# Performance work log

Hardware: AMD Instinct MI355X
Metric: run time of the kernel (lower is better)

Reference implementation:

```python
import jax, jax.numpy as jnp
import numpy as np

N = 50000
E = 800000
IN_DIM = 128
HIDDEN = 96
HEADS = 4
HEAD_DIM = HIDDEN // HEADS
NUM_LAYERS = 3
NEG_SLOPE = 0.2


def _gat_layer(h, W, a_l, a_r, b, src, dst):
    # h: [N, F_in], W: [F_in, H*D], a_l/a_r: [H, D], b: [H, D]
    feat = (h @ W).reshape(N, HEADS, HEAD_DIM)          # [N, H, D]
    el = jnp.sum(feat * a_l, axis=-1)                    # [N, H]
    er = jnp.sum(feat * a_r, axis=-1)                    # [N, H]
    e = el[src] + er[dst]                                # [E, H]
    e = jnp.where(e > 0, e, NEG_SLOPE * e)               # leaky_relu
    # edge softmax over incoming edges of each dst node
    m = jax.ops.segment_max(e, dst, num_segments=N)      # [N, H]
    ex = jnp.exp(e - m[dst])                             # [E, H]
    denom = jax.ops.segment_sum(ex, dst, num_segments=N) # [N, H]
    alpha = ex / denom[dst]                              # [E, H]
    msg = feat[src] * alpha[:, :, None]                  # [E, H, D]
    out = jax.ops.segment_sum(msg, dst, num_segments=N)  # [N, H, D]
    out = out + b                                        # bias
    out = jax.nn.elu(out)                                # activation
    return out.reshape(N, HEADS * HEAD_DIM)              # flatten(1)


def setup_inputs() -> dict:
    key = jax.random.key(0)
    ks = jax.random.split(key, 16)
    feats = jax.random.normal(ks[0], (N, IN_DIM), dtype=jnp.float32)
    src = jax.random.randint(ks[1], (E,), 0, N)
    dst = jax.random.randint(ks[2], (E,), 0, N)
    inp = {"feats": feats, "src": src, "dst": dst}
    fin = IN_DIM
    for l in range(NUM_LAYERS):
        s = 1.0 / np.sqrt(fin)
        inp[f"W{l}"] = jax.random.normal(ks[3 + 4 * l], (fin, HIDDEN), dtype=jnp.float32) * s
        inp[f"al{l}"] = jax.random.normal(ks[4 + 4 * l], (HEADS, HEAD_DIM), dtype=jnp.float32) * 0.1
        inp[f"ar{l}"] = jax.random.normal(ks[5 + 4 * l], (HEADS, HEAD_DIM), dtype=jnp.float32) * 0.1
        inp[f"b{l}"] = jnp.zeros((HEADS, HEAD_DIM), dtype=jnp.float32)
        fin = HIDDEN
    return inp


def reference(feats, src, dst, W0, al0, ar0, b0, W1, al1, ar1, b1, W2, al2, ar2, b2):
    h = feats
    params = [(W0, al0, ar0, b0), (W1, al1, ar1, b1), (W2, al2, ar2, b2)]
    for (W, al, ar, b) in params:
        h = _gat_layer(h, W, al, ar, b, src, dst)
    # AvgPooling over all nodes (single graph) -> [1, HIDDEN]
    return jnp.mean(h, axis=0, keepdims=True)
```

## Files before the change

### kernel.cpp

```cpp
#include <hip/hip_runtime.h>
#include <hip/hip_bf16.h>

#define N_NODES 50000
#define E_EDGES 800000
#define IN_DIM  128
#define HIDDEN  96
#define HEADS   4
#define HEAD_DIM 24
#define NEG_SLOPE 0.2f
#define POOL_BLOCKS 256


__global__ void k_hist(const int* __restrict__ dst, int* __restrict__ deg) {
    int e = blockIdx.x * 256 + threadIdx.x;
    if (e < E_EDGES) atomicAdd(&deg[dst[e]], 1);
}

__global__ __launch_bounds__(256) void k_scan1(const int* __restrict__ deg,
                                               int* __restrict__ bsum, int n) {
    int i = blockIdx.x * 256 + threadIdx.x;
    int v = (i < n) ? deg[i] : 0;
#pragma unroll
    for (int s = 1; s < 64; s <<= 1) v += __shfl_xor(v, s);
    __shared__ int ws[4];
    if ((threadIdx.x & 63) == 0) ws[threadIdx.x >> 6] = v;
    __syncthreads();
    if (threadIdx.x == 0) bsum[blockIdx.x] = ws[0] + ws[1] + ws[2] + ws[3];
}

__global__ __launch_bounds__(256) void k_scan3(const int* __restrict__ deg,
                                               const int* __restrict__ bsum,
                                               int* __restrict__ off, int n) {
    int tid = threadIdx.x;
    int lane = tid & 63, wv = tid >> 6;

    int pv = (tid < blockIdx.x) ? bsum[tid] : 0;
#pragma unroll
    for (int s = 1; s < 64; s <<= 1) pv += __shfl_xor(pv, s);

    int i = blockIdx.x * 256 + tid;
    int v = (i < n) ? deg[i] : 0;
    int x = v;
#pragma unroll
    for (int s = 1; s < 64; s <<= 1) {
        int t = __shfl_up(x, s);
        if (lane >= s) x += t;
    }

    __shared__ int wsum[4], wsum2[4];
    if (lane == 63) wsum[wv] = x;
    if (lane == 0)  wsum2[wv] = pv;
    __syncthreads();
    int add = wsum2[0] + wsum2[1] + wsum2[2] + wsum2[3];
    for (int w = 0; w < wv; ++w) add += wsum[w];
    if (i < n) off[i] = x - v + add;
    if (i == n - 1) off[n] = x + add;
}

__global__ void k_fill(const int* __restrict__ src, const int* __restrict__ dst,
                       const int* __restrict__ off, int* __restrict__ cursor,
                       int* __restrict__ ssrc) {
    int e = blockIdx.x * 256 + threadIdx.x;
    if (e < E_EDGES) {
        int d = dst[e];
        int p = off[d] + atomicAdd(&cursor[d], 1);
        ssrc[p] = src[e];
    }
}


template <int K>
__global__ __launch_bounds__(384) void k_gemm(const float* __restrict__ h,
                                              const float* __restrict__ W,
                                              const float* __restrict__ al_g,
                                              const float* __restrict__ ar_g,
                                              float* __restrict__ feat,
                                              float* __restrict__ el,
                                              float* __restrict__ er, int n) {
    constexpr int HL = 64 * K;
    constexpr int PT = 384 * 17;
    constexpr int SM = (HL > PT) ? HL : PT;
    __shared__ float smem[SM];
    float* hl = smem;

    int node0 = blockIdx.x * 64;
    int total4 = 64 * K / 4;
    for (int idx = threadIdx.x; idx < total4; idx += 384) {
        int node = idx / (K / 4);
        int koff = (idx % (K / 4)) * 4;
        float4 v = make_float4(0.f, 0.f, 0.f, 0.f);
        if (node0 + node < n)
            v = *(const float4*)(&h[(size_t)(node0 + node) * K + koff]);
        *(float4*)(&hl[node * K + koff]) = v;
    }
    __syncthreads();
    int grp = threadIdx.x / 48;
    int c = (threadIdx.x % 48) * 2;
    int nb = grp * 8;
    float acc[8][2];
#pragma unroll
    for (int i = 0; i < 8; ++i) acc[i][0] = acc[i][1] = 0.f;
    for (int k = 0; k < K; k += 4) {
        float2 w0 = *(const float2*)&W[(k + 0) * 96 + c];
        float2 w1 = *(const float2*)&W[(k + 1) * 96 + c];
        float2 w2 = *(const float2*)&W[(k + 2) * 96 + c];
        float2 w3 = *(const float2*)&W[(k + 3) * 96 + c];
#pragma unroll
        for (int i = 0; i < 8; ++i) {
            float4 hv = *(const float4*)&hl[(nb + i) * K + k];
            acc[i][0] = fmaf(hv.x, w0.x, acc[i][0]);
            acc[i][1] = fmaf(hv.x, w0.y, acc[i][1]);
            acc[i][0] = fmaf(hv.y, w1.x, acc[i][0]);
            acc[i][1] = fmaf(hv.y, w1.y, acc[i][1]);
            acc[i][0] = fmaf(hv.z, w2.x, acc[i][0]);
            acc[i][1] = fmaf(hv.z, w2.y, acc[i][1]);
            acc[i][0] = fmaf(hv.w, w3.x, acc[i][0]);
            acc[i][1] = fmaf(hv.w, w3.y, acc[i][1]);
        }
    }
#pragma unroll
    for (int i = 0; i < 8; ++i) {
        int node = node0 + nb + i;
        if (node < n) *(float2*)&feat[(size_t)node * 96 + c] = make_float2(acc[i][0], acc[i][1]);
    }
    float alc0 = al_g[c], alc1 = al_g[c + 1];
    float arc0 = ar_g[c], arc1 = ar_g[c + 1];
    __syncthreads();
    float* part = smem;
    int base = threadIdx.x * 17;
#pragma unroll
    for (int i = 0; i < 8; ++i) {
        part[base + i * 2]     = acc[i][0] * alc0 + acc[i][1] * alc1;
        part[base + i * 2 + 1] = acc[i][0] * arc0 + acc[i][1] * arc1;
    }
    __syncthreads();
    if (threadIdx.x < 256) {
        int ig = threadIdx.x >> 2;
        int hh = threadIdx.x & 3;
        int g2 = ig >> 3, il = ig & 7;
        float se = 0.f, sr = 0.f;
#pragma unroll
        for (int cc = 0; cc < 12; ++cc) {
            int t = g2 * 48 + hh * 12 + cc;
            se += part[t * 17 + il * 2];
            sr += part[t * 17 + il * 2 + 1];
        }
        int node = node0 + ig;
        if (node < n) {
            el[node * 4 + hh] = se;
            er[node * 4 + hh] = sr;
        }
    }
}

__global__ __launch_bounds__(256) void k_agg(const int* __restrict__ off,
                                             const int* __restrict__ ssrc,
                                             const float* __restrict__ el,
                                             const float* __restrict__ er,
                                             const float* __restrict__ feat,
                                             const float* __restrict__ bias,
                                             float* __restrict__ out) {
    int n = blockIdx.x * 4 + (threadIdx.x >> 6);
    if (n >= N_NODES) return;
    int lane = threadIdx.x & 63;
    int j0   = lane >> 3;
    int h    = (lane >> 1) & 3;
    int half = lane & 1;
    int cbase = h * 24 + half * 12;
    unsigned cboff = (unsigned)cbase * 4u;

    int start = off[n], deg = off[n + 1] - start;
    float er_h = er[(unsigned)n * 4u + h];

    float e_reg[4];
    unsigned s_reg[4];
    float lmax = -1e30f;
#pragma unroll
    for (int t = 0; t < 4; ++t) {
        int j = t * 8 + j0;
        bool act = (j < deg);
        unsigned s = act ? (unsigned)ssrc[start + j] : 0u;
        float e = -1e30f;
        if (act) {
            e = el[s * 4u + h] + er_h;
            e = (e > 0.f) ? e : NEG_SLOPE * e;
        }
        s_reg[t] = s;
        e_reg[t] = e;
        lmax = fmaxf(lmax, e);
    }
    for (int j = 32 + j0; j < deg; j += 8) {
        unsigned s = (unsigned)ssrc[start + j];
        float e = el[s * 4u + h] + er_h;
        e = (e > 0.f) ? e : NEG_SLOPE * e;
        lmax = fmaxf(lmax, e);
    }
    lmax = fmaxf(lmax, __shfl_xor(lmax, 8));
    lmax = fmaxf(lmax, __shfl_xor(lmax, 16));
    lmax = fmaxf(lmax, __shfl_xor(lmax, 32));
    float m = lmax;

    float acc[12];
#pragma unroll
    for (int c = 0; c < 12; ++c) acc[c] = 0.f;
    float den = 0.f;
#pragma unroll
    for (int t = 0; t < 4; ++t) {
        int j = t * 8 + j0;
        if (j < deg) {
            float ex = __expf(e_reg[t] - m);
            den += ex;
            const float* fr = (const float*)((const char*)feat + (size_t)(s_reg[t] * 384u + cboff));
            float4 v0 = *(const float4*)(fr + 0);
            float4 v1 = *(const float4*)(fr + 4);
            float4 v2 = *(const float4*)(fr + 8);
            acc[0] = fmaf(ex, v0.x, acc[0]);  acc[1] = fmaf(ex, v0.y, acc[1]);
            acc[2] = fmaf(ex, v0.z, acc[2]);  acc[3] = fmaf(ex, v0.w, acc[3]);
            acc[4] = fmaf(ex, v1.x, acc[4]);  acc[5] = fmaf(ex, v1.y, acc[5]);
            acc[6] = fmaf(ex, v1.z, acc[6]);  acc[7] = fmaf(ex, v1.w, acc[7]);
            acc[8] = fmaf(ex, v2.x, acc[8]);  acc[9] = fmaf(ex, v2.y, acc[9]);
            acc[10] = fmaf(ex, v2.z, acc[10]); acc[11] = fmaf(ex, v2.w, acc[11]);
        }
    }
    for (int j = 32 + j0; j < deg; j += 8) {
        unsigned s = (unsigned)ssrc[start + j];
        float e = el[s * 4u + h] + er_h;
        e = (e > 0.f) ? e : NEG_SLOPE * e;
        float ex = __expf(e - m);
        den += ex;
        const float* fr = (const float*)((const char*)feat + (size_t)(s * 384u + cboff));
        float4 v0 = *(const float4*)(fr + 0);
        float4 v1 = *(const float4*)(fr + 4);
        float4 v2 = *(const float4*)(fr + 8);
        acc[0] = fmaf(ex, v0.x, acc[0]);  acc[1] = fmaf(ex, v0.y, acc[1]);
        acc[2] = fmaf(ex, v0.z, acc[2]);  acc[3] = fmaf(ex, v0.w, acc[3]);
        acc[4] = fmaf(ex, v1.x, acc[4]);  acc[5] = fmaf(ex, v1.y, acc[5]);
        acc[6] = fmaf(ex, v1.z, acc[6]);  acc[7] = fmaf(ex, v1.w, acc[7]);
        acc[8] = fmaf(ex, v2.x, acc[8]);  acc[9] = fmaf(ex, v2.y, acc[9]);
        acc[10] = fmaf(ex, v2.z, acc[10]); acc[11] = fmaf(ex, v2.w, acc[11]);
    }

#pragma unroll
    for (int st = 8; st <= 32; st <<= 1) {
        den += __shfl_xor(den, st);
#pragma unroll
        for (int c = 0; c < 12; ++c) acc[c] += __shfl_xor(acc[c], st);
    }

    if (j0 == 0) {
        float rden = (den > 0.f) ? 1.f / den : 0.f;
        const float* bp = &bias[cbase];
        float o[12];
#pragma unroll
        for (int c = 0; c < 12; ++c) {
            float v = acc[c] * rden + bp[c];
            o[c] = (v > 0.f) ? v : (__expf(v) - 1.f);
        }
        float* op = &out[(size_t)n * 96 + cbase];
        *(float4*)(op + 0) = make_float4(o[0], o[1], o[2], o[3]);
        *(float4*)(op + 4) = make_float4(o[4], o[5], o[6], o[7]);
        *(float4*)(op + 8) = make_float4(o[8], o[9], o[10], o[11]);
    }
}

__global__ __launch_bounds__(384) void k_pool1(const float* __restrict__ h,
                                               float* __restrict__ partial) {
    int r = threadIdx.x / 96;
    int c = threadIdx.x % 96;
    float a = 0.f;
    for (int nrow = blockIdx.x * 4 + r; nrow < N_NODES; nrow += POOL_BLOCKS * 4)
        a += h[(size_t)nrow * 96 + c];
    __shared__ float sred[4][96];
    sred[r][c] = a;
    __syncthreads();
    if (r == 0)
        partial[blockIdx.x * 96 + c] = sred[0][c] + sred[1][c] + sred[2][c] + sred[3][c];
}

__global__ __launch_bounds__(384) void k_pool2(const float* __restrict__ partial,
                                               float* __restrict__ out) {
    int g = threadIdx.x / 96;
    int c = threadIdx.x % 96;
    float a = 0.f;
    for (int b = g; b < POOL_BLOCKS; b += 4)
        a += partial[b * 96 + c];
    __shared__ float sred[4][96];
    sred[g][c] = a;
    __syncthreads();
    if (g == 0)
        out[c] = (sred[0][c] + sred[1][c] + sred[2][c] + sred[3][c]) * (1.0f / N_NODES);
}


extern "C" void kernel_launch(void* const* d_in, const int* in_sizes, int n_in,
                              void* d_out, int out_size, void* d_ws, size_t ws_size,
                              hipStream_t stream) {
    const float* feats = (const float*)d_in[0];
    const int* src = (const int*)d_in[1];
    const int* dst = (const int*)d_in[2];

    char* p = (char*)d_ws;
    auto alloc = [&](size_t bytes) {
        void* r = (void*)p;
        p += (bytes + 255) & ~(size_t)255;
        return r;
    };
    float* A       = (float*)alloc((size_t)N_NODES * 96 * 4);
    float* B       = (float*)alloc((size_t)N_NODES * 96 * 4);
    float* el      = (float*)alloc((size_t)N_NODES * 4 * 4);
    float* er      = (float*)alloc((size_t)N_NODES * 4 * 4);
    int* degcur    = (int*)alloc((size_t)N_NODES * 2 * 4);
    int* off       = (int*)alloc((size_t)(N_NODES + 1) * 4);
    int* bsum      = (int*)alloc((size_t)256 * 4);
    int* ssrc      = (int*)alloc((size_t)E_EDGES * 4);
    float* partial = (float*)alloc((size_t)POOL_BLOCKS * 96 * 4);
    int* deg = degcur;
    int* cursor = degcur + N_NODES;

    hipMemsetAsync(degcur, 0, (size_t)N_NODES * 2 * 4, stream);

    const int NB = (N_NODES + 255) / 256;
    k_hist<<<(E_EDGES + 255) / 256, 256, 0, stream>>>(dst, deg);
    k_scan1<<<NB, 256, 0, stream>>>(deg, bsum, N_NODES);
    k_scan3<<<NB, 256, 0, stream>>>(deg, bsum, off, N_NODES);
    k_fill<<<(E_EDGES + 255) / 256, 256, 0, stream>>>(src, dst, off, cursor, ssrc);

    const float* hin = feats;
    for (int l = 0; l < 3; ++l) {
        const float* W  = (const float*)d_in[3 + 4 * l];
        const float* al = (const float*)d_in[4 + 4 * l];
        const float* ar = (const float*)d_in[5 + 4 * l];
        const float* bb = (const float*)d_in[6 + 4 * l];

        if (l == 0)
            k_gemm<IN_DIM><<<(N_NODES + 63) / 64, 384, 0, stream>>>(hin, W, al, ar, B, el, er, N_NODES);
        else
            k_gemm<HIDDEN><<<(N_NODES + 63) / 64, 384, 0, stream>>>(hin, W, al, ar, B, el, er, N_NODES);

        k_agg<<<(N_NODES + 3) / 4, 256, 0, stream>>>(off, ssrc, el, er, B, bb, A);
        hin = A;
    }

    k_pool1<<<POOL_BLOCKS, 384, 0, stream>>>(A, partial);
    k_pool2<<<1, 384, 0, stream>>>(partial, (float*)d_out);
}
```

Before: 439.5 us.

## Store projected features in fp16 and merge scan and pooling kernels

The projected features written by the GEMM are stored as fp16 and converted back to float in the aggregation kernel, which halves the bytes gathered per edge. The two-pass scan is folded into one kernel in which each block re-sums all earlier degrees. The two-stage pooling reduction is replaced by atomic adds into an output that the histogram kernel zeroes first. This removes two launches at the cost of fp16 rounding error, redundant prefix reads and non-deterministic float atomics.

New measurement: 420.5 us. 1.05x faster.

```diff
diff --git a/kernel.cpp b/kernel.cpp
--- a/kernel.cpp
+++ b/kernel.cpp
@@ -1,44 +1,31 @@
 #include <hip/hip_runtime.h>
-#include <hip/hip_bf16.h>
+#include <hip/hip_fp16.h>
 
 #define N_NODES 50000
 #define E_EDGES 800000
 #define IN_DIM  128
 #define HIDDEN  96
-#define HEADS   4
-#define HEAD_DIM 24
 #define NEG_SLOPE 0.2f
 #define POOL_BLOCKS 256
 
 
-__global__ void k_hist(const int* __restrict__ dst, int* __restrict__ deg) {
+__global__ void k_hist(const int* __restrict__ dst, int* __restrict__ deg,
+                       float* __restrict__ out) {
+    if (blockIdx.x == 0 && threadIdx.x < 96) out[threadIdx.x] = 0.f;
     int e = blockIdx.x * 256 + threadIdx.x;
     if (e < E_EDGES) atomicAdd(&deg[dst[e]], 1);
 }
 
-__global__ __launch_bounds__(256) void k_scan1(const int* __restrict__ deg,
-                                               int* __restrict__ bsum, int n) {
-    int i = blockIdx.x * 256 + threadIdx.x;
-    int v = (i < n) ? deg[i] : 0;
-#pragma unroll
-    for (int s = 1; s < 64; s <<= 1) v += __shfl_xor(v, s);
-    __shared__ int ws[4];
-    if ((threadIdx.x & 63) == 0) ws[threadIdx.x >> 6] = v;
-    __syncthreads();
-    if (threadIdx.x == 0) bsum[blockIdx.x] = ws[0] + ws[1] + ws[2] + ws[3];
-}
-
-__global__ __launch_bounds__(256) void k_scan3(const int* __restrict__ deg,
-                                               const int* __restrict__ bsum,
-                                               int* __restrict__ off, int n) {
+__global__ __launch_bounds__(256) void k_scan(const int* __restrict__ deg,
+                                              int* __restrict__ off, int n) {
     int tid = threadIdx.x;
     int lane = tid & 63, wv = tid >> 6;
-
-    int pv = (tid < blockIdx.x) ? bsum[tid] : 0;
+    int base = blockIdx.x * 256;
+    int pv = 0;
+    for (int i = tid; i < base; i += 256) pv += deg[i];
 #pragma unroll
     for (int s = 1; s < 64; s <<= 1) pv += __shfl_xor(pv, s);
-
-    int i = blockIdx.x * 256 + tid;
+    int i = base + tid;
     int v = (i < n) ? deg[i] : 0;
     int x = v;
 #pragma unroll
@@ -46,12 +33,11 @@
         int t = __shfl_up(x, s);
         if (lane >= s) x += t;
     }
-
-    __shared__ int wsum[4], wsum2[4];
+    __shared__ int wsum[4], psum[4];
     if (lane == 63) wsum[wv] = x;
-    if (lane == 0)  wsum2[wv] = pv;
-    __syncthreads();
-    int add = wsum2[0] + wsum2[1] + wsum2[2] + wsum2[3];
+    if (lane == 0)  psum[wv] = pv;
+    __syncthreads();
+    int add = psum[0] + psum[1] + psum[2] + psum[3];
     for (int w = 0; w < wv; ++w) add += wsum[w];
     if (i < n) off[i] = x - v + add;
     if (i == n - 1) off[n] = x + add;
@@ -74,7 +60,7 @@
                                               const float* __restrict__ W,
                                               const float* __restrict__ al_g,
                                               const float* __restrict__ ar_g,
-                                              float* __restrict__ feat,
+                                              __half* __restrict__ feat,
                                               float* __restrict__ el,
                                               float* __restrict__ er, int n) {
     constexpr int HL = 64 * K;
@@ -121,7 +107,9 @@
 #pragma unroll
     for (int i = 0; i < 8; ++i) {
         int node = node0 + nb + i;
-        if (node < n) *(float2*)&feat[(size_t)node * 96 + c] = make_float2(acc[i][0], acc[i][1]);
+        if (node < n)
+            *(__half2*)&feat[(size_t)node * 96 + c] =
+                __floats2half2_rn(acc[i][0], acc[i][1]);
     }
     float alc0 = al_g[c], alc1 = al_g[c + 1];
     float arc0 = ar_g[c], arc1 = ar_g[c + 1];
@@ -157,7 +145,7 @@
                                              const int* __restrict__ ssrc,
                                              const float* __restrict__ el,
                                              const float* __restrict__ er,
-                                             const float* __restrict__ feat,
+                                             const __half* __restrict__ feat,
                                              const float* __restrict__ bias,
                                              float* __restrict__ out) {
     int n = blockIdx.x * 4 + (threadIdx.x >> 6);
@@ -167,7 +155,7 @@
     int h    = (lane >> 1) & 3;
     int half = lane & 1;
     int cbase = h * 24 + half * 12;
-    unsigned cboff = (unsigned)cbase * 4u;
+    unsigned cboff = (unsigned)cbase * 2u;
 
     int start = off[n], deg = off[n + 1] - start;
     float er_h = er[(unsigned)n * 4u + h];
@@ -210,16 +198,20 @@
         if (j < deg) {
             float ex = __expf(e_reg[t] - m);
             den += ex;
-            const float* fr = (const float*)((const char*)feat + (size_t)(s_reg[t] * 384u + cboff));
-            float4 v0 = *(const float4*)(fr + 0);
-            float4 v1 = *(const float4*)(fr + 4);
-            float4 v2 = *(const float4*)(fr + 8);
-            acc[0] = fmaf(ex, v0.x, acc[0]);  acc[1] = fmaf(ex, v0.y, acc[1]);
-            acc[2] = fmaf(ex, v0.z, acc[2]);  acc[3] = fmaf(ex, v0.w, acc[3]);
-            acc[4] = fmaf(ex, v1.x, acc[4]);  acc[5] = fmaf(ex, v1.y, acc[5]);
-            acc[6] = fmaf(ex, v1.z, acc[6]);  acc[7] = fmaf(ex, v1.w, acc[7]);
-            acc[8] = fmaf(ex, v2.x, acc[8]);  acc[9] = fmaf(ex, v2.y, acc[9]);
-            acc[10] = fmaf(ex, v2.z, acc[10]); acc[11] = fmaf(ex, v2.w, acc[11]);
+            const __half2* fr = (const __half2*)((const char*)feat +
+                                  (size_t)(s_reg[t] * 192u + cboff));
+            float2 f0 = __half22float2(fr[0]);
+            float2 f1 = __half22float2(fr[1]);
+            float2 f2 = __half22float2(fr[2]);
+            float2 f3 = __half22float2(fr[3]);
+            float2 f4 = __half22float2(fr[4]);
+            float2 f5 = __half22float2(fr[5]);
+            acc[0] = fmaf(ex, f0.x, acc[0]);   acc[1] = fmaf(ex, f0.y, acc[1]);
+            acc[2] = fmaf(ex, f1.x, acc[2]);   acc[3] = fmaf(ex, f1.y, acc[3]);
+            acc[4] = fmaf(ex, f2.x, acc[4]);   acc[5] = fmaf(ex, f2.y, acc[5]);
+            acc[6] = fmaf(ex, f3.x, acc[6]);   acc[7] = fmaf(ex, f3.y, acc[7]);
+            acc[8] = fmaf(ex, f4.x, acc[8]);   acc[9] = fmaf(ex, f4.y, acc[9]);
+            acc[10] = fmaf(ex, f5.x, acc[10]); acc[11] = fmaf(ex, f5.y, acc[11]);
         }
     }
     for (int j = 32 + j0; j < deg; j += 8) {
@@ -228,16 +220,20 @@
         e = (e > 0.f) ? e : NEG_SLOPE * e;
         float ex = __expf(e - m);
         den += ex;
-        const float* fr = (const float*)((const char*)feat + (size_t)(s * 384u + cboff));
-        float4 v0 = *(const float4*)(fr + 0);
-        float4 v1 = *(const float4*)(fr + 4);
-        float4 v2 = *(const float4*)(fr + 8);
-        acc[0] = fmaf(ex, v0.x, acc[0]);  acc[1] = fmaf(ex, v0.y, acc[1]);
-        acc[2] = fmaf(ex, v0.z, acc[2]);  acc[3] = fmaf(ex, v0.w, acc[3]);
-        acc[4] = fmaf(ex, v1.x, acc[4]);  acc[5] = fmaf(ex, v1.y, acc[5]);
-        acc[6] = fmaf(ex, v1.z, acc[6]);  acc[7] = fmaf(ex, v1.w, acc[7]);
-        acc[8] = fmaf(ex, v2.x, acc[8]);  acc[9] = fmaf(ex, v2.y, acc[9]);
-        acc[10] = fmaf(ex, v2.z, acc[10]); acc[11] = fmaf(ex, v2.w, acc[11]);
+        const __half2* fr = (const __half2*)((const char*)feat +
+                              (size_t)(s * 192u + cboff));
+        float2 f0 = __half22float2(fr[0]);
+        float2 f1 = __half22float2(fr[1]);
+        float2 f2 = __half22float2(fr[2]);
+        float2 f3 = __half22float2(fr[3]);
+        float2 f4 = __half22float2(fr[4]);
+        float2 f5 = __half22float2(fr[5]);
+        acc[0] = fmaf(ex, f0.x, acc[0]);   acc[1] = fmaf(ex, f0.y, acc[1]);
+        acc[2] = fmaf(ex, f1.x, acc[2]);   acc[3] = fmaf(ex, f1.y, acc[3]);
+        acc[4] = fmaf(ex, f2.x, acc[4]);   acc[5] = fmaf(ex, f2.y, acc[5]);
+        acc[6] = fmaf(ex, f3.x, acc[6]);   acc[7] = fmaf(ex, f3.y, acc[7]);
+        acc[8] = fmaf(ex, f4.x, acc[8]);   acc[9] = fmaf(ex, f4.y, acc[9]);
+        acc[10] = fmaf(ex, f5.x, acc[10]); acc[11] = fmaf(ex, f5.y, acc[11]);
     }
 
 #pragma unroll
@@ -263,8 +259,8 @@
     }
 }
 
-__global__ __launch_bounds__(384) void k_pool1(const float* __restrict__ h,
-                                               float* __restrict__ partial) {
+__global__ __launch_bounds__(384) void k_pool(const float* __restrict__ h,
+                                              float* __restrict__ out) {
     int r = threadIdx.x / 96;
     int c = threadIdx.x % 96;
     float a = 0.f;
@@ -274,21 +270,8 @@
     sred[r][c] = a;
     __syncthreads();
     if (r == 0)
-        partial[blockIdx.x * 96 + c] = sred[0][c] + sred[1][c] + sred[2][c] + sred[3][c];
-}
-
-__global__ __launch_bounds__(384) void k_pool2(const float* __restrict__ partial,
-                                               float* __restrict__ out) {
-    int g = threadIdx.x / 96;
-    int c = threadIdx.x % 96;
-    float a = 0.f;
-    for (int b = g; b < POOL_BLOCKS; b += 4)
-        a += partial[b * 96 + c];
-    __shared__ float sred[4][96];
-    sred[g][c] = a;
-    __syncthreads();
-    if (g == 0)
-        out[c] = (sred[0][c] + sred[1][c] + sred[2][c] + sred[3][c]) * (1.0f / N_NODES);
+        atomicAdd(&out[c],
+                  (sred[0][c] + sred[1][c] + sred[2][c] + sred[3][c]) * (1.0f / N_NODES));
 }
 
 
@@ -305,24 +288,21 @@
         p += (bytes + 255) & ~(size_t)255;
         return r;
     };
-    float* A       = (float*)alloc((size_t)N_NODES * 96 * 4);
-    float* B       = (float*)alloc((size_t)N_NODES * 96 * 4);
-    float* el      = (float*)alloc((size_t)N_NODES * 4 * 4);
-    float* er      = (float*)alloc((size_t)N_NODES * 4 * 4);
+    float*  A      = (float*)alloc((size_t)N_NODES * 96 * 4);
+    __half* B      = (__half*)alloc((size_t)N_NODES * 96 * 2);
+    float*  el     = (float*)alloc((size_t)N_NODES * 4 * 4);
+    float*  er     = (float*)alloc((size_t)N_NODES * 4 * 4);
     int* degcur    = (int*)alloc((size_t)N_NODES * 2 * 4);
     int* off       = (int*)alloc((size_t)(N_NODES + 1) * 4);
-    int* bsum      = (int*)alloc((size_t)256 * 4);
     int* ssrc      = (int*)alloc((size_t)E_EDGES * 4);
-    float* partial = (float*)alloc((size_t)POOL_BLOCKS * 96 * 4);
     int* deg = degcur;
     int* cursor = degcur + N_NODES;
 
     hipMemsetAsync(degcur, 0, (size_t)N_NODES * 2 * 4, stream);
 
     const int NB = (N_NODES + 255) / 256;
-    k_hist<<<(E_EDGES + 255) / 256, 256, 0, stream>>>(dst, deg);
-    k_scan1<<<NB, 256, 0, stream>>>(deg, bsum, N_NODES);
-    k_scan3<<<NB, 256, 0, stream>>>(deg, bsum, off, N_NODES);
+    k_hist<<<(E_EDGES + 255) / 256, 256, 0, stream>>>(dst, deg, (float*)d_out);
+    k_scan<<<NB, 256, 0, stream>>>(deg, off, N_NODES);
     k_fill<<<(E_EDGES + 255) / 256, 256, 0, stream>>>(src, dst, off, cursor, ssrc);
 
     const float* hin = feats;
@@ -341,6 +321,5 @@
         hin = A;
     }
 
-    k_pool1<<<POOL_BLOCKS, 384, 0, stream>>>(A, partial);
-    k_pool2<<<1, 384, 0, stream>>>(partial, (float*)d_out);
-}
+    k_pool<<<POOL_BLOCKS, 384, 0, stream>>>(A, (float*)d_out);
+}
```
